# Performance work log

Measured on AMD Instinct MI355X. Metric: run time of the kernel, lower is better.

Reference implementation:

```python
import jax, jax.numpy as jnp
import numpy as np
import math

N_HEADS = 16
HEAD_DIM = 64
D_MODEL = 1024
B, S = 2, 2048


def setup_inputs() -> dict:
    key = jax.random.key(0)
    ks = jax.random.split(key, 12)
    Dh = N_HEADS * HEAD_DIM
    sc = 1.0 / math.sqrt(D_MODEL)
    return {
        "will_be_queries": jax.random.normal(ks[0], (B, S, D_MODEL), jnp.float32),
        "will_be_keys": jax.random.normal(ks[1], (B, S, D_MODEL), jnp.float32),
        "will_be_values": jax.random.normal(ks[2], (B, S, D_MODEL), jnp.float32),
        "valid_len": jax.random.randint(ks[3], (B,), 1, S + 1, jnp.int32),
        # torch nn.Linear weights: (out_features, in_features)
        "w_q": jax.random.normal(ks[4], (Dh, D_MODEL), jnp.float32) * sc,
        "b_q": jnp.zeros((Dh,), jnp.float32),
        "w_k": jax.random.normal(ks[5], (Dh, D_MODEL), jnp.float32) * sc,
        "b_k": jnp.zeros((Dh,), jnp.float32),
        "w_v": jax.random.normal(ks[6], (Dh, D_MODEL), jnp.float32) * sc,
        "b_v": jnp.zeros((Dh,), jnp.float32),
        "w_o": jax.random.normal(ks[7], (D_MODEL, Dh), jnp.float32) * sc,
        "b_o": jnp.zeros((D_MODEL,), jnp.float32),
    }


def _split_heads(x):
    # (B, S, H*Dh) -> (B, H, S, Dh)
    b, s, _ = x.shape
    return x.reshape(b, s, N_HEADS, HEAD_DIM).transpose(0, 2, 1, 3)


def reference(will_be_queries, will_be_keys, will_be_values, valid_len,
              w_q, b_q, w_k, b_k, w_v, b_v, w_o, b_o):
    q = _split_heads(will_be_queries @ w_q.T + b_q)   # (B,H,S,Dh)
    k = _split_heads(will_be_keys @ w_k.T + b_k)
    v = _split_heads(will_be_values @ w_v.T + b_v)

    scores = jnp.einsum("bhqd,bhkd->bhqk", q, k) / jnp.sqrt(
        jnp.asarray(HEAD_DIM, q.dtype))

    neg = jnp.finfo(scores.dtype).min
    q_idx = jnp.arange(scores.shape[2])[:, None]   # (S,1)
    k_idx = jnp.arange(scores.shape[3])[None, :]   # (1,S)
    causal = k_idx > q_idx                         # look-ahead mask (offset=1 triu)
    vmask = k_idx[None] >= valid_len[:, None, None]  # (B,S,S) keys beyond valid_len
    mask = causal[None, None] | vmask[:, None]       # (B,1|H,S,S) broadcast over heads
    scores = jnp.where(mask, neg, scores)

    attn = jax.nn.softmax(scores, axis=-1)
    out = jnp.einsum("bhqk,bhkd->bhqd", attn, v)   # (B,H,S,Dh)
    out = out.transpose(0, 2, 1, 3).reshape(out.shape[0], out.shape[2], N_HEADS * HEAD_DIM)
    return out @ w_o.T + b_o
```

## Files before the change

### kernel.cpp

```cpp
#include <hip/hip_runtime.h>
#include <math.h>

#define NH 16
#define HD 64
#define DM 1024
#define BB 2
#define SS 2048
#define MROWS (BB*SS)
#define MEG 1048576

typedef __attribute__((ext_vector_type(8))) short bf16x8;
typedef __attribute__((ext_vector_type(4))) float f32x4;

__device__ __forceinline__ unsigned short f2bf(float x) {
    unsigned int u = __float_as_uint(x);
    u += 0x7fff + ((u >> 16) & 1);
    return (unsigned short)(u >> 16);
}

#define GLD_LDS16(gp, lp) __builtin_amdgcn_global_load_lds(                  \
        (const __attribute__((address_space(1))) void*)(gp),                 \
        (__attribute__((address_space(3))) void*)(lp), 16, 0, 0)

__global__ __launch_bounds__(256)
void cvt_all(const float* __restrict__ xq, const float* __restrict__ xk,
             const float* __restrict__ xv, const float* __restrict__ wq,
             const float* __restrict__ wk, const float* __restrict__ wv,
             const float* __restrict__ wo, unsigned short* __restrict__ ws)
{
    const int reg = blockIdx.y;
    const size_t n    = (reg < 3) ? (size_t)4 * MEG : (size_t)MEG;
    const size_t roff = (reg < 3) ? (size_t)reg * 4 * MEG
                                  : (size_t)12 * MEG + (size_t)(reg - 3) * MEG;
    const float* src = (reg == 0) ? xq : (reg == 1) ? xk : (reg == 2) ? xv :
                       (reg == 3) ? wq : (reg == 4) ? wk : (reg == 5) ? wv : wo;
    const size_t i = ((size_t)blockIdx.x * 256 + threadIdx.x) * 8;
    if (i >= n) return;
    const float4 a = *(const float4*)(src + i);
    const float4 b = *(const float4*)(src + i + 4);
    ushort4 lo4, hi4;
    lo4.x = f2bf(a.x); lo4.y = f2bf(a.y); lo4.z = f2bf(a.z); lo4.w = f2bf(a.w);
    hi4.x = f2bf(b.x); hi4.y = f2bf(b.y); hi4.z = f2bf(b.z); hi4.w = f2bf(b.w);
    *(ushort4*)(ws + roff + i)     = lo4;
    *(ushort4*)(ws + roff + i + 4) = hi4;
}

template<int MODE>
__device__ __forceinline__ void gemm_mfma_core(
    const unsigned short* __restrict__ A,
    const unsigned short* __restrict__ W,
    const float* __restrict__ bias,
    void* __restrict__ Y, int ldy,
    unsigned short* __restrict__ As,
    unsigned short* __restrict__ Bs)
{
    const int tid  = threadIdx.x;
    const int w    = tid >> 6;
    const int lane = tid & 63;
    const int lo   = lane & 15;
    const int g    = lane >> 4;
    const int wr   = (w >> 1) * 64;
    const int wc   = (w & 1) * 64;

    f32x4 acc[4][4];
#pragma unroll
    for (int i = 0; i < 4; ++i)
#pragma unroll
        for (int j = 0; j < 4; ++j) acc[i][j] = (f32x4)0.f;

    for (int k0 = 0; k0 < 1024; k0 += 64) {
        __syncthreads();
#pragma unroll
        for (int u = 0; u < 4; ++u) {
            const int ci  = u * 256 + tid;
            const int row = ci >> 3, c = ci & 7;
            const int sc  = (c ^ (row & 7)) * 8;
            GLD_LDS16(A + (size_t)row * 1024 + k0 + sc, As + ci * 8);
            GLD_LDS16(W + (size_t)row * 1024 + k0 + sc, Bs + ci * 8);
        }
        asm volatile("s_waitcnt vmcnt(0)" ::: "memory");
        __syncthreads();

#pragma unroll
        for (int kk = 0; kk < 2; ++kk) {
            bf16x8 af[4], bf[4];
#pragma unroll
            for (int i = 0; i < 4; ++i) {
                const int ra = wr + i * 16 + lo;
                const int rb = wc + i * 16 + lo;
                af[i] = *(const bf16x8*)(As + ra * 64 + (((kk * 4 + g) ^ (ra & 7)) * 8));
                bf[i] = *(const bf16x8*)(Bs + rb * 64 + (((kk * 4 + g) ^ (rb & 7)) * 8));
            }
#pragma unroll
            for (int i = 0; i < 4; ++i)
#pragma unroll
                for (int j = 0; j < 4; ++j)
                    acc[i][j] = __builtin_amdgcn_mfma_f32_16x16x32_bf16(
                        af[i], bf[j], acc[i][j], 0, 0, 0);
        }
    }

#pragma unroll
    for (int i = 0; i < 4; ++i) {
#pragma unroll
        for (int j = 0; j < 4; ++j) {
            const int col = wc + j * 16 + lo;
#pragma unroll
            for (int r = 0; r < 4; ++r) {
                const int row = wr + i * 16 + g * 4 + r;
                if constexpr (MODE == 2) {
                    const float v = acc[i][j][r] + bias[row];
                    const int jc = (col & ~63) | ((((col >> 3) & 7) ^ (row & 7)) << 3)
                                 | (col & 7);
                    ((unsigned short*)Y)[(size_t)row * ldy + jc] = f2bf(v);
                } else {
                    const float v = acc[i][j][r] + bias[col];
                    if constexpr (MODE == 0)
                        ((unsigned short*)Y)[(size_t)row * ldy + col] = f2bf(v);
                    else
                        ((float*)Y)[(size_t)row * ldy + col] = v;
                }
            }
        }
    }
}

__global__ __launch_bounds__(256)
void qkv_proj(const unsigned short* __restrict__ ws,
              const float* __restrict__ bq, const float* __restrict__ bk,
              const float* __restrict__ bv,
              unsigned short* __restrict__ qk, unsigned short* __restrict__ vt)
{
    __shared__ unsigned short As[128 * 64];
    __shared__ unsigned short Bs[128 * 64];
    const int wg   = blockIdx.x;
    const int flat = (wg & 7) * 96 + (wg >> 3);
    const int fg   = flat >> 3;
    const int sub  = flat & 7;
    const int mat  = fg >> 5;
    const int r    = fg & 31;
    if (mat < 2) {
        const int m0   = r * 128;
        const int ncol = sub * 128;
        const unsigned short* A = ws + (size_t)mat * 4 * MEG + (size_t)m0 * 1024;
        const unsigned short* W = ws + (size_t)12 * MEG + (size_t)mat * MEG
                                     + (size_t)ncol * 1024;
        const float* bias = ((mat == 0) ? bq : bk) + ncol;
        gemm_mfma_core<0>(A, W, bias,
                          qk + (size_t)m0 * 2048 + mat * 1024 + ncol, 2048, As, Bs);
    } else {
        const int b      = r >> 4;
        const int colblk = r & 15;
        const int rowblk = sub;
        const unsigned short* A = ws + (size_t)14 * MEG + (size_t)rowblk * 128 * 1024;
        const unsigned short* W = ws + (size_t)8 * MEG + (size_t)b * 2 * MEG
                                     + (size_t)colblk * 128 * 1024;
        gemm_mfma_core<2>(A, W, bv + rowblk * 128,
                          vt + (size_t)b * 1024 * 2048
                             + (size_t)rowblk * 128 * 2048 + colblk * 128, 2048,
                          As, Bs);
    }
}

__global__ __launch_bounds__(256)
void out_proj(const unsigned short* __restrict__ ws,
              const float* __restrict__ bo, float* __restrict__ out)
{
    __shared__ unsigned short As[128 * 64];
    __shared__ unsigned short Bs[128 * 64];
    const int wg   = blockIdx.x;
    const int flat = (wg & 7) * 32 + (wg >> 3);
    const int m0   = (flat >> 3) * 128;
    const int n0   = (flat & 7) * 128;
    const unsigned short* A = ws + (size_t)28 * MEG + (size_t)m0 * 1024;
    const unsigned short* W = ws + (size_t)15 * MEG + (size_t)n0 * 1024;
    gemm_mfma_core<1>(A, W, bo + n0, out + (size_t)m0 * 1024 + n0, 1024, As, Bs);
}

__global__ __launch_bounds__(256)
void attn_mfma(const unsigned short* __restrict__ qk,
               const unsigned short* __restrict__ vt,
               const int* __restrict__ vlen, unsigned short* __restrict__ aout)
{
    __shared__ unsigned short Ks[2][64 * 64];
    __shared__ unsigned short Vs[2][64 * 64];
    __shared__ unsigned short Ps[4][16 * 64];

    const int bh  = blockIdx.x;
    const int qt  = 31 - blockIdx.y;
    const int b   = bh >> 4;
    const int h   = bh & 15;
    const int q0  = qt * 64;
    const int vl  = vlen[b];
    const int tid = threadIdx.x;
    const int w    = tid >> 6;
    const int lane = tid & 63;
    const int lo   = lane & 15;
    const int g    = lane >> 4;
    const int lx   = lo & 7;

    const unsigned short* qbase = qk + (size_t)(b * SS) * 2048 + h * 64;
    const unsigned short* kbase = qbase + 1024;
    const unsigned short* vtb   = vt + (size_t)b * 1024 * 2048
                                     + (size_t)(h * 64) * 2048;

    const int qg = q0 + w * 16 + lo;
    const bf16x8 a0 = *(const bf16x8*)(qbase + (size_t)qg * 2048 + g * 8);
    const bf16x8 a1 = *(const bf16x8*)(qbase + (size_t)qg * 2048 + 32 + g * 8);

    float mR = -INFINITY, lR = 0.f;
    f32x4 of[4];
#pragma unroll
    for (int f = 0; f < 4; ++f) of[f] = (f32x4)0.f;

    const int kmax   = min(q0 + 64, vl);
    const int ntiles = (kmax + 63) >> 6;

#pragma unroll
    for (int u = 0; u < 2; ++u) {
        const int e = w * 128 + u * 64 + lane;
        const int r = e >> 3, c = e & 7;
        GLD_LDS16(kbase + (size_t)r * 2048 + ((c ^ (r & 7)) * 8), &Ks[0][e * 8]);
        GLD_LDS16(vtb + (size_t)r * 2048 + c * 8, &Vs[0][e * 8]);
    }

    unsigned short* const Psw = Ps[w];

    for (int kt = 0; kt < ntiles; ++kt) {
        const int cur = kt & 1;
        const int k0  = kt * 64;
        if (kt + 1 < ntiles) {
            const int kn = k0 + 64;
#pragma unroll
            for (int u = 0; u < 2; ++u) {
                const int e = w * 128 + u * 64 + lane;
                const int r = e >> 3, c = e & 7;
                GLD_LDS16(kbase + (size_t)(kn + r) * 2048 + ((c ^ (r & 7)) * 8),
                          &Ks[cur ^ 1][e * 8]);
                GLD_LDS16(vtb + (size_t)r * 2048 + kn + c * 8, &Vs[cur ^ 1][e * 8]);
            }
            asm volatile("s_waitcnt vmcnt(4)" ::: "memory");
        } else {
            asm volatile("s_waitcnt vmcnt(0)" ::: "memory");
        }
        __syncthreads();

        f32x4 sf[4];
#pragma unroll
        for (int f = 0; f < 4; ++f) sf[f] = (f32x4)0.f;
        __builtin_amdgcn_s_setprio(1);
#pragma unroll
        for (int f = 0; f < 4; ++f) {
            const int kr = f * 16 + lo;
            const bf16x8 kb0 = *(const bf16x8*)(&Ks[cur][kr * 64 + ((g ^ lx) * 8)]);
            const bf16x8 kb1 = *(const bf16x8*)(&Ks[cur][kr * 64 + (((4 + g) ^ lx) * 8)]);
            sf[f] = __builtin_amdgcn_mfma_f32_16x16x32_bf16(kb0, a0, sf[f], 0, 0, 0);
            sf[f] = __builtin_amdgcn_mfma_f32_16x16x32_bf16(kb1, a1, sf[f], 0, 0, 0);
        }
        __builtin_amdgcn_s_setprio(0);

        const bool full = (k0 + 63 <= q0 + w * 16) && (k0 + 64 <= vl);
        float sv[16];
        float t = -INFINITY;
#pragma unroll
        for (int f = 0; f < 4; ++f)
#pragma unroll
            for (int r = 0; r < 4; ++r) {
                float x = sf[f][r] * 0.125f;
                if (!full) {
                    const int kg = k0 + f * 16 + g * 4 + r;
                    x = (kg <= qg && kg < vl) ? x : -INFINITY;
                }
                sv[f * 4 + r] = x;
                t = fmaxf(t, x);
            }
        t = fmaxf(t, __shfl_xor(t, 16));
        t = fmaxf(t, __shfl_xor(t, 32));

        if (!__all(t <= mR + 8.f)) {
            const float mn   = fmaxf(mR, t);
            const float corr = __expf(mR - mn);
            lR *= corr;
#pragma unroll
            for (int f = 0; f < 4; ++f)
#pragma unroll
                for (int r = 0; r < 4; ++r) of[f][r] *= corr;
            mR = mn;
        }

        float ps = 0.f;
#pragma unroll
        for (int f = 0; f < 4; ++f) {
            const float p0 = __expf(sv[f * 4 + 0] - mR);
            const float p1 = __expf(sv[f * 4 + 1] - mR);
            const float p2 = __expf(sv[f * 4 + 2] - mR);
            const float p3 = __expf(sv[f * 4 + 3] - mR);
            ps += (p0 + p1) + (p2 + p3);
            ushort4 pk;
            pk.x = f2bf(p0); pk.y = f2bf(p1); pk.z = f2bf(p2); pk.w = f2bf(p3);
            *(ushort4*)(Psw + lo * 64 + (((f * 2 + (g >> 1)) ^ lx) * 8)
                        + (g & 1) * 4) = pk;
        }
        ps += __shfl_xor(ps, 16);
        ps += __shfl_xor(ps, 32);
        lR += ps;

        __builtin_amdgcn_s_setprio(1);
#pragma unroll
        for (int kk = 0; kk < 2; ++kk) {
            const bf16x8 pa = *(const bf16x8*)(Psw + lo * 64 + (((kk * 4 + g) ^ lx) * 8));
#pragma unroll
            for (int f = 0; f < 4; ++f) {
                const bf16x8 vb = *(const bf16x8*)(&Vs[cur][(f * 16 + lo) * 64
                                    + (((4 * kk + g) ^ lx) * 8)]);
                of[f] = __builtin_amdgcn_mfma_f32_16x16x32_bf16(vb, pa, of[f], 0, 0, 0);
            }
        }
        __builtin_amdgcn_s_setprio(0);
        __syncthreads();
    }

    const float rv = 1.0f / lR;
    unsigned short* ob = aout + (size_t)(b * SS + q0 + w * 16 + lo) * 1024 + h * 64;
#pragma unroll
    for (int f = 0; f < 4; ++f) {
        ushort4 ov;
        ov.x = f2bf(of[f][0] * rv);
        ov.y = f2bf(of[f][1] * rv);
        ov.z = f2bf(of[f][2] * rv);
        ov.w = f2bf(of[f][3] * rv);
        *(ushort4*)(ob + f * 16 + g * 4) = ov;
    }
}

extern "C" void kernel_launch(void* const* d_in, const int* in_sizes, int n_in,
                              void* d_out, int out_size, void* d_ws, size_t ws_size,
                              hipStream_t stream) {
    const float* xq = (const float*)d_in[0];
    const float* xk = (const float*)d_in[1];
    const float* xv = (const float*)d_in[2];
    const int*   vl = (const int*)  d_in[3];
    const float* wq = (const float*)d_in[4];
    const float* bq = (const float*)d_in[5];
    const float* wk = (const float*)d_in[6];
    const float* bk = (const float*)d_in[7];
    const float* wv = (const float*)d_in[8];
    const float* bv = (const float*)d_in[9];
    const float* wo = (const float*)d_in[10];
    const float* bo = (const float*)d_in[11];

    unsigned short* ws     = (unsigned short*)d_ws;
    unsigned short* qkbuf  = ws + (size_t)16 * MEG;
    unsigned short* vtbuf  = ws + (size_t)24 * MEG;
    unsigned short* abuf   = ws + (size_t)28 * MEG;

    cvt_all<<<dim3(2048, 7), 256, 0, stream>>>(xq, xk, xv, wq, wk, wv, wo, ws);
    qkv_proj<<<dim3(768), 256, 0, stream>>>(ws, bq, bk, bv, qkbuf, vtbuf);
    attn_mfma<<<dim3(BB * NH, SS / 64), 256, 0, stream>>>(qkbuf, vtbuf, vl, abuf);
    out_proj<<<dim3(256), 256, 0, stream>>>(ws, bo, (float*)d_out);
}
```

Baseline: 125.9 us.

## Interleave causal attention tile order across heads and use exp2 softmax

```diff
diff --git a/kernel.cpp b/kernel.cpp
--- a/kernel.cpp
+++ b/kernel.cpp
@@ -16,6 +16,10 @@
     unsigned int u = __float_as_uint(x);
     u += 0x7fff + ((u >> 16) & 1);
     return (unsigned short)(u >> 16);
+}
+
+__device__ __forceinline__ unsigned int pack2bf(float a, float b) {
+    return (unsigned int)f2bf(a) | ((unsigned int)f2bf(b) << 16);
 }
 
 #define GLD_LDS16(gp, lp) __builtin_amdgcn_global_load_lds(                  \
@@ -186,12 +190,15 @@
     __shared__ unsigned short Vs[2][64 * 64];
     __shared__ unsigned short Ps[4][16 * 64];
 
-    const int bh  = blockIdx.x;
-    const int qt  = 31 - blockIdx.y;
-    const int b   = bh >> 4;
-    const int h   = bh & 15;
-    const int q0  = qt * 64;
-    const int vl  = vlen[b];
+    const int x = blockIdx.x, y = blockIdx.y;
+    const int j = y & 7, t4 = y >> 3;
+    const int qt = (t4 == 0) ? j : (t4 == 1) ? (15 - j)
+                 : (t4 == 2) ? (16 + j) : (31 - j);
+    const int bh = (x + y) & 31;
+    const int b  = bh >> 4;
+    const int h  = bh & 15;
+    const int q0 = qt * 64;
+    const int vl = vlen[b];
     const int tid = threadIdx.x;
     const int w    = tid >> 6;
     const int lane = tid & 63;
@@ -225,6 +232,7 @@
     }
 
     unsigned short* const Psw = Ps[w];
+    const float SC = 0.125f * 1.44269504f;
 
     for (int kt = 0; kt < ntiles; ++kt) {
         const int cur = kt & 1;
@@ -261,25 +269,29 @@
 
         const bool full = (k0 + 63 <= q0 + w * 16) && (k0 + 64 <= vl);
         float sv[16];
-        float t = -INFINITY;
 #pragma unroll
         for (int f = 0; f < 4; ++f)
 #pragma unroll
             for (int r = 0; r < 4; ++r) {
-                float x = sf[f][r] * 0.125f;
+                float xv = sf[f][r] * SC;
                 if (!full) {
                     const int kg = k0 + f * 16 + g * 4 + r;
-                    x = (kg <= qg && kg < vl) ? x : -INFINITY;
+                    xv = (kg <= qg && kg < vl) ? xv : -INFINITY;
                 }
-                sv[f * 4 + r] = x;
-                t = fmaxf(t, x);
-            }
+                sv[f * 4 + r] = xv;
+            }
+        float t0 = fmaxf(fmaxf(sv[0],  sv[1]),  sv[2]);
+        float t1 = fmaxf(fmaxf(sv[3],  sv[4]),  sv[5]);
+        float t2 = fmaxf(fmaxf(sv[6],  sv[7]),  sv[8]);
+        float t3 = fmaxf(fmaxf(sv[9],  sv[10]), sv[11]);
+        float t4m = fmaxf(fmaxf(sv[12], sv[13]), sv[14]);
+        float t = fmaxf(fmaxf(fmaxf(t0, t1), fmaxf(t2, t3)), fmaxf(t4m, sv[15]));
         t = fmaxf(t, __shfl_xor(t, 16));
         t = fmaxf(t, __shfl_xor(t, 32));
 
-        if (!__all(t <= mR + 8.f)) {
+        if (!__all(t <= mR + 11.54f)) {
             const float mn   = fmaxf(mR, t);
-            const float corr = __expf(mR - mn);
+            const float corr = exp2f(mR - mn);
             lR *= corr;
 #pragma unroll
             for (int f = 0; f < 4; ++f)
@@ -291,15 +303,16 @@
         float ps = 0.f;
 #pragma unroll
         for (int f = 0; f < 4; ++f) {
-            const float p0 = __expf(sv[f * 4 + 0] - mR);
-            const float p1 = __expf(sv[f * 4 + 1] - mR);
-            const float p2 = __expf(sv[f * 4 + 2] - mR);
-            const float p3 = __expf(sv[f * 4 + 3] - mR);
+            const float p0 = exp2f(sv[f * 4 + 0] - mR);
+            const float p1 = exp2f(sv[f * 4 + 1] - mR);
+            const float p2 = exp2f(sv[f * 4 + 2] - mR);
+            const float p3 = exp2f(sv[f * 4 + 3] - mR);
             ps += (p0 + p1) + (p2 + p3);
-            ushort4 pk;
-            pk.x = f2bf(p0); pk.y = f2bf(p1); pk.z = f2bf(p2); pk.w = f2bf(p3);
-            *(ushort4*)(Psw + lo * 64 + (((f * 2 + (g >> 1)) ^ lx) * 8)
-                        + (g & 1) * 4) = pk;
+            uint2 pw;
+            pw.x = pack2bf(p0, p1);
+            pw.y = pack2bf(p2, p3);
+            *(uint2*)(Psw + lo * 64 + (((f * 2 + (g >> 1)) ^ lx) * 8)
+                      + (g & 1) * 4) = pw;
         }
         ps += __shfl_xor(ps, 16);
         ps += __shfl_xor(ps, 32);
```

New measurement: 132.0 us. 1.05x slower.
